# Optimization experiments

Measured on AMD Instinct MI355X. Metric: run time of the kernel, lower is better.

## Reference

```python
import jax, jax.numpy as jnp
import numpy as np

N_NODES = 100000


def gcn_conv(x, src, dst, W, b, n_nodes):
    # PyG GCNConv: add self-loops, sym-normalize, transform then aggregate.
    loop = jnp.arange(n_nodes, dtype=src.dtype)
    s = jnp.concatenate([src, loop])
    d = jnp.concatenate([dst, loop])
    ones = jnp.ones(s.shape[0], dtype=x.dtype)
    deg = jax.ops.segment_sum(ones, d, num_segments=n_nodes)
    dinv = jnp.where(deg > 0, jax.lax.rsqrt(deg), 0.0)
    norm = dinv[s] * dinv[d]  # [E+N]
    h = x @ W                 # [N, out]
    msg = h[s] * norm[:, None]
    out = jax.ops.segment_sum(msg, d, num_segments=n_nodes)
    return out + b


def setup_inputs() -> dict:
    key = jax.random.key(0)
    ks = jax.random.split(key, 10)
    n, f = N_NODES, 128
    x = jax.random.normal(ks[0], (n, f), dtype=jnp.float32)
    edge_index = jax.random.randint(ks[1], (2, 1600000), 0, n, dtype=jnp.int64)

    def glorot(k, fin, fout):
        lim = float(np.sqrt(6.0 / (fin + fout)))
        return jax.random.uniform(k, (fin, fout), jnp.float32, -lim, lim)

    return {
        "x": x,
        "edge_index": edge_index,
        "W1": glorot(ks[2], f, 128), "b1": jnp.zeros((128,), jnp.float32),
        "W2": glorot(ks[3], 128, 64), "b2": jnp.zeros((64,), jnp.float32),
        "W3": glorot(ks[4], 64, 32), "b3": jnp.zeros((32,), jnp.float32),
        "Wc": glorot(ks[5], 64, 1), "bc": jnp.zeros((1,), jnp.float32),
    }


def reference(x, edge_index, W1, b1, W2, b2, W3, b3, Wc, bc):
    n = x.shape[0]
    src, dst = edge_index[0], edge_index[1]
    h = jax.nn.relu(gcn_conv(x, src, dst, W1, b1, n))   # dropout: eval mode
    h = jax.nn.relu(gcn_conv(h, src, dst, W2, b2, n))
    h = jax.nn.relu(gcn_conv(h, src, dst, W3, b3, n))
    edge_feat = jnp.concatenate([h[src], h[dst]], axis=1)  # [E, 64]
    return edge_feat @ Wc + bc
```

## Files before the change

kernel.cpp:

```cpp
#include <hip/hip_runtime.h>


typedef unsigned short u16;
typedef short bfrag __attribute__((ext_vector_type(8)));
typedef float ffrag __attribute__((ext_vector_type(4)));

#define BSHIFT 8
#define MAXB   512
#define BIN_CHUNK 4096
#define BCAP   4608

static __device__ __forceinline__ float4 f4add(float4 a, float4 b) {
    return make_float4(a.x + b.x, a.y + b.y, a.z + b.z, a.w + b.w);
}

static __device__ __forceinline__ u16 f2bf(float f) {
    unsigned u = __float_as_uint(f);
    u = (u + 0x7FFFu + ((u >> 16) & 1u)) >> 16;
    return (u16)u;
}

static __device__ __forceinline__ float bflo(unsigned u) {
    return __uint_as_float(u << 16);
}
static __device__ __forceinline__ float bfhi(unsigned u) {
    return __uint_as_float(u & 0xFFFF0000u);
}
static __device__ __forceinline__ void bfacc2(float& a0, float& a1, unsigned u) {
    a0 += bflo(u);
    a1 += bfhi(u);
}
static __device__ __forceinline__ void bfacc8(float* a, uint4 u) {
    bfacc2(a[0], a[1], u.x); bfacc2(a[2], a[3], u.y);
    bfacc2(a[4], a[5], u.z); bfacc2(a[6], a[7], u.w);
}


__global__ __launch_bounds__(256) void bin_edges(const int* __restrict__ src,
                                                 const int* __restrict__ dst,
                                                 int* __restrict__ bcur,
                                                 unsigned* __restrict__ pairs,
                                                 int E, int B) {
    __shared__ int h[MAXB];
    __shared__ int base[MAXB];
    const int t = threadIdx.x;
    const int e0 = blockIdx.x * BIN_CHUNK;
    const int eEnd = min(e0 + BIN_CHUNK, E);
    for (int i = t; i < B; i += 256) h[i] = 0;
    __syncthreads();
    for (int e = e0 + t; e < eEnd; e += 256)
        atomicAdd(&h[dst[e] >> BSHIFT], 1);
    __syncthreads();
    for (int i = t; i < B; i += 256) {
        int c = h[i];
        base[i] = c ? atomicAdd(&bcur[i], c) : 0;
        h[i] = 0;
    }
    __syncthreads();
    for (int e = e0 + t; e < eEnd; e += 256) {
        int d = dst[e];
        int b = d >> BSHIFT;
        int pos = base[b] + atomicAdd(&h[b], 1);
        pairs[pos] = ((unsigned)(d & 255) << 24) | (unsigned)src[e];
    }
}

__global__ __launch_bounds__(256) void build_csr(const unsigned* __restrict__ pairs,
                                                 const int* __restrict__ bcur,
                                                 int* __restrict__ rowp,
                                                 int* __restrict__ rowe,
                                                 float* __restrict__ dinv,
                                                 int* __restrict__ ssrc, int N) {
    __shared__ int s[256];
    __shared__ int cur[256];
    const int t = threadIdx.x;
    const int b = blockIdx.x;
    const int eBeg = b * BCAP, eEnd = bcur[b];
    const int nodeBase = b << BSHIFT;
    s[t] = 0;
    __syncthreads();
    for (int e = eBeg + t; e < eEnd; e += 256)
        atomicAdd(&s[pairs[e] >> 24], 1);
    __syncthreads();
    const int v = s[t];
    #pragma unroll
    for (int off = 1; off < 256; off <<= 1) {
        int add = (t >= off) ? s[t - off] : 0;
        __syncthreads();
        s[t] += add;
        __syncthreads();
    }
    const int rp = eBeg + s[t] - v;
    const int node = nodeBase + t;
    if (node < N) {
        rowp[node] = rp;
        rowe[node] = rp + v;
        dinv[node] = rsqrtf((float)(v + 1));
    }
    cur[t] = rp;
    __syncthreads();
    for (int e = eBeg + t; e < eEnd; e += 256) {
        unsigned p = pairs[e];
        int pos = atomicAdd(&cur[p >> 24], 1);
        ssrc[pos] = (int)(p & 0xFFFFFFu);
    }
}

__global__ __launch_bounds__(256) void prep_all(const float* __restrict__ W1,
                                                u16* __restrict__ w1t,
                                                const float* __restrict__ W2,
                                                u16* __restrict__ w2t,
                                                int* __restrict__ bcur, int B) {
    int idx = blockIdx.x * 256 + threadIdx.x;
    if (idx < 128 * 128) {
        int n = idx >> 7, k = idx & 127;
        w1t[idx] = f2bf(W1[k * 128 + n]);
    } else if (idx < 128 * 128 + 64 * 128) {
        int j = idx - 128 * 128;
        int n = j >> 7, k = j & 127;
        w2t[j] = f2bf(W2[k * 64 + n]);
    }
    if (idx < B) bcur[idx] = idx * BCAP;
}

template <int FIN, int FOUT, bool AF32, int MINW>
__global__ __launch_bounds__(256, MINW)
void gemm_mfma(const void* __restrict__ Xv, const u16* __restrict__ Wt,
               const float* __restrict__ dinv, u16* __restrict__ G, int N) {
    constexpr int NT = FOUT / 16;
    constexpr int KK = FIN / 32;
    constexpr int CB = FIN / 8;
    constexpr int ITER = (64 * CB) / 256;
    __shared__ __align__(16) u16 xs[64 * FIN];
    __shared__ float ldv[64];

    const int t = threadIdx.x;
    const int wave = t >> 6;
    const int lane = t & 63;
    const int l15 = lane & 15;
    const int quad = lane >> 4;
    const int r0 = blockIdx.x * 64;

    bfrag Bf[NT][KK];
    #pragma unroll
    for (int nt = 0; nt < NT; nt++)
        #pragma unroll
        for (int kk = 0; kk < KK; kk++)
            Bf[nt][kk] = *reinterpret_cast<const bfrag*>(
                &Wt[(size_t)(nt * 16 + l15) * FIN + kk * 32 + quad * 8]);

    if (t < 64) ldv[t] = (r0 + t < N) ? dinv[r0 + t] : 0.f;

    #pragma unroll
    for (int i = 0; i < ITER; i++) {
        int v = t + 256 * i;
        int row = v / CB;
        int cb = v - row * CB;
        uint4 pack = make_uint4(0, 0, 0, 0);
        if (r0 + row < N) {
            if (AF32) {
                const float* X = (const float*)Xv;
                const float4* p = reinterpret_cast<const float4*>(
                    &X[(size_t)(r0 + row) * FIN + cb * 8]);
                float4 lo = p[0], hi = p[1];
                pack.x = f2bf(lo.x) | ((unsigned)f2bf(lo.y) << 16);
                pack.y = f2bf(lo.z) | ((unsigned)f2bf(lo.w) << 16);
                pack.z = f2bf(hi.x) | ((unsigned)f2bf(hi.y) << 16);
                pack.w = f2bf(hi.z) | ((unsigned)f2bf(hi.w) << 16);
            } else {
                const u16* X = (const u16*)Xv;
                pack = *reinterpret_cast<const uint4*>(
                    &X[(size_t)(r0 + row) * FIN + cb * 8]);
            }
        }
        int cbs = cb ^ (row & 7);
        *reinterpret_cast<uint4*>(&xs[row * FIN + cbs * 8]) = pack;
    }
    __syncthreads();

    ffrag acc[NT];
    #pragma unroll
    for (int nt = 0; nt < NT; nt++) {
        acc[nt][0] = 0.f; acc[nt][1] = 0.f; acc[nt][2] = 0.f; acc[nt][3] = 0.f;
    }

    const int arow = wave * 16 + l15;
    #pragma unroll
    for (int kk = 0; kk < KK; kk++) {
        int cb = (kk * 4 + quad) ^ (l15 & 7);
        bfrag a = *reinterpret_cast<const bfrag*>(&xs[arow * FIN + cb * 8]);
        #pragma unroll
        for (int nt = 0; nt < NT; nt++)
            acc[nt] = __builtin_amdgcn_mfma_f32_16x16x32_bf16(a, Bf[nt][kk], acc[nt], 0, 0, 0);
    }

    #pragma unroll
    for (int nt = 0; nt < NT; nt++)
        #pragma unroll
        for (int r = 0; r < 4; r++) {
            int rl = wave * 16 + quad * 4 + r;
            int grow = r0 + rl;
            if (grow < N)
                G[(size_t)grow * FOUT + nt * 16 + l15] = f2bf(acc[nt][r] * ldv[rl]);
        }
}

__global__ __launch_bounds__(256) void agg1_gemm2(const u16* __restrict__ G,
                                                  const int* __restrict__ rowp,
                                                  const int* __restrict__ rowe,
                                                  const int* __restrict__ ssrc,
                                                  const float* __restrict__ dinv,
                                                  const float* __restrict__ bias,
                                                  const u16* __restrict__ w2t,
                                                  u16* __restrict__ g2, int N) {
    __shared__ __align__(16) u16 hl[16][136];
    __shared__ float ldv[16];
    const int t = threadIdx.x;
    const int wave = t >> 6;
    const int lane = t & 63;
    const int l15 = lane & 15;
    const int quad = lane >> 4;
    const int lj = t & 15;
    const int dn = t >> 4;
    const int d0 = blockIdx.x * 16;
    const int d = d0 + dn;

    if (t < 16) ldv[t] = (d0 + t < N) ? dinv[d0 + t] : 0.f;

    uint4 pk = make_uint4(0, 0, 0, 0);
    if (d < N) {
        const uint4* G4 = reinterpret_cast<const uint4*>(G);
        float a[8];
        #pragma unroll
        for (int i = 0; i < 8; i++) a[i] = 0.f;
        bfacc8(a, G4[(size_t)d * 16 + lj]);
        int e = rowp[d];
        const int end = rowe[d];
        for (; e + 8 <= end; e += 8) {
            int s0 = ssrc[e],     s1 = ssrc[e + 1], s2 = ssrc[e + 2], s3 = ssrc[e + 3];
            int s4 = ssrc[e + 4], s5 = ssrc[e + 5], s6 = ssrc[e + 6], s7 = ssrc[e + 7];
            uint4 u0 = G4[(size_t)s0 * 16 + lj];
            uint4 u1 = G4[(size_t)s1 * 16 + lj];
            uint4 u2 = G4[(size_t)s2 * 16 + lj];
            uint4 u3 = G4[(size_t)s3 * 16 + lj];
            uint4 u4 = G4[(size_t)s4 * 16 + lj];
            uint4 u5 = G4[(size_t)s5 * 16 + lj];
            uint4 u6 = G4[(size_t)s6 * 16 + lj];
            uint4 u7 = G4[(size_t)s7 * 16 + lj];
            bfacc8(a, u0); bfacc8(a, u1); bfacc8(a, u2); bfacc8(a, u3);
            bfacc8(a, u4); bfacc8(a, u5); bfacc8(a, u6); bfacc8(a, u7);
        }
        for (; e + 4 <= end; e += 4) {
            int s0 = ssrc[e], s1 = ssrc[e + 1], s2 = ssrc[e + 2], s3 = ssrc[e + 3];
            uint4 u0 = G4[(size_t)s0 * 16 + lj];
            uint4 u1 = G4[(size_t)s1 * 16 + lj];
            uint4 u2 = G4[(size_t)s2 * 16 + lj];
            uint4 u3 = G4[(size_t)s3 * 16 + lj];
            bfacc8(a, u0); bfacc8(a, u1); bfacc8(a, u2); bfacc8(a, u3);
        }
        for (; e < end; e++)
            bfacc8(a, G4[(size_t)ssrc[e] * 16 + lj]);
        const float dv = dinv[d];
        const float4 b0 = reinterpret_cast<const float4*>(bias)[lj * 2];
        const float4 b1 = reinterpret_cast<const float4*>(bias)[lj * 2 + 1];
        float h[8];
        h[0] = fmaxf(a[0] * dv + b0.x, 0.f);
        h[1] = fmaxf(a[1] * dv + b0.y, 0.f);
        h[2] = fmaxf(a[2] * dv + b0.z, 0.f);
        h[3] = fmaxf(a[3] * dv + b0.w, 0.f);
        h[4] = fmaxf(a[4] * dv + b1.x, 0.f);
        h[5] = fmaxf(a[5] * dv + b1.y, 0.f);
        h[6] = fmaxf(a[6] * dv + b1.z, 0.f);
        h[7] = fmaxf(a[7] * dv + b1.w, 0.f);
        pk.x = f2bf(h[0]) | ((unsigned)f2bf(h[1]) << 16);
        pk.y = f2bf(h[2]) | ((unsigned)f2bf(h[3]) << 16);
        pk.z = f2bf(h[4]) | ((unsigned)f2bf(h[5]) << 16);
        pk.w = f2bf(h[6]) | ((unsigned)f2bf(h[7]) << 16);
    }
    *reinterpret_cast<uint4*>(&hl[dn][lj * 8]) = pk;
    __syncthreads();

    bfrag Bf[4];
    #pragma unroll
    for (int kk = 0; kk < 4; kk++)
        Bf[kk] = *reinterpret_cast<const bfrag*>(
            &w2t[(size_t)(wave * 16 + l15) * 128 + kk * 32 + quad * 8]);

    ffrag acc;
    acc[0] = 0.f; acc[1] = 0.f; acc[2] = 0.f; acc[3] = 0.f;
    #pragma unroll
    for (int kk = 0; kk < 4; kk++) {
        bfrag av = *reinterpret_cast<const bfrag*>(&hl[l15][kk * 32 + quad * 8]);
        acc = __builtin_amdgcn_mfma_f32_16x16x32_bf16(av, Bf[kk], acc, 0, 0, 0);
    }
    #pragma unroll
    for (int r = 0; r < 4; r++) {
        int row = quad * 4 + r;
        int node = d0 + row;
        if (node < N)
            g2[(size_t)node * 64 + wave * 16 + l15] = f2bf(acc[r] * ldv[row]);
    }
}

__global__ __launch_bounds__(256) void agg2_gemm3(const u16* __restrict__ G,
                                                  const int* __restrict__ rowp,
                                                  const int* __restrict__ rowe,
                                                  const int* __restrict__ ssrc,
                                                  const float* __restrict__ dinv,
                                                  const float* __restrict__ bias,
                                                  const float* __restrict__ W3,
                                                  float* __restrict__ g3, int N) {
    __shared__ __align__(16) float wl[64 * 32];
    __shared__ __align__(16) float hl[32][68];
    const int t = threadIdx.x;
    {
        const float4* s4 = reinterpret_cast<const float4*>(W3);
        float4* d4 = reinterpret_cast<float4*>(wl);
        d4[t] = s4[t];
        d4[t + 256] = s4[t + 256];
    }
    __syncthreads();
    const int lj = t & 7;
    const int dn = t >> 3;
    const int d = blockIdx.x * 32 + dn;
    if (d >= N) return;

    const uint4* G4 = reinterpret_cast<const uint4*>(G);
    float a[8];
    #pragma unroll
    for (int i = 0; i < 8; i++) a[i] = 0.f;
    bfacc8(a, G4[(size_t)d * 8 + lj]);
    int e = rowp[d];
    const int end = rowe[d];
    for (; e + 8 <= end; e += 8) {
        int s0 = ssrc[e],     s1 = ssrc[e + 1], s2 = ssrc[e + 2], s3 = ssrc[e + 3];
        int s4 = ssrc[e + 4], s5 = ssrc[e + 5], s6 = ssrc[e + 6], s7 = ssrc[e + 7];
        uint4 u0 = G4[(size_t)s0 * 8 + lj];
        uint4 u1 = G4[(size_t)s1 * 8 + lj];
        uint4 u2 = G4[(size_t)s2 * 8 + lj];
        uint4 u3 = G4[(size_t)s3 * 8 + lj];
        uint4 u4 = G4[(size_t)s4 * 8 + lj];
        uint4 u5 = G4[(size_t)s5 * 8 + lj];
        uint4 u6 = G4[(size_t)s6 * 8 + lj];
        uint4 u7 = G4[(size_t)s7 * 8 + lj];
        bfacc8(a, u0); bfacc8(a, u1); bfacc8(a, u2); bfacc8(a, u3);
        bfacc8(a, u4); bfacc8(a, u5); bfacc8(a, u6); bfacc8(a, u7);
    }
    for (; e + 4 <= end; e += 4) {
        int s0 = ssrc[e], s1 = ssrc[e + 1], s2 = ssrc[e + 2], s3 = ssrc[e + 3];
        uint4 u0 = G4[(size_t)s0 * 8 + lj];
        uint4 u1 = G4[(size_t)s1 * 8 + lj];
        uint4 u2 = G4[(size_t)s2 * 8 + lj];
        uint4 u3 = G4[(size_t)s3 * 8 + lj];
        bfacc8(a, u0); bfacc8(a, u1); bfacc8(a, u2); bfacc8(a, u3);
    }
    for (; e < end; e++)
        bfacc8(a, G4[(size_t)ssrc[e] * 8 + lj]);
    const float dv = dinv[d];
    const float4 b0 = reinterpret_cast<const float4*>(bias)[lj * 2];
    const float4 b1 = reinterpret_cast<const float4*>(bias)[lj * 2 + 1];
    float h[8];
    h[0] = fmaxf(a[0] * dv + b0.x, 0.f);
    h[1] = fmaxf(a[1] * dv + b0.y, 0.f);
    h[2] = fmaxf(a[2] * dv + b0.z, 0.f);
    h[3] = fmaxf(a[3] * dv + b0.w, 0.f);
    h[4] = fmaxf(a[4] * dv + b1.x, 0.f);
    h[5] = fmaxf(a[5] * dv + b1.y, 0.f);
    h[6] = fmaxf(a[6] * dv + b1.z, 0.f);
    h[7] = fmaxf(a[7] * dv + b1.w, 0.f);
    *reinterpret_cast<float4*>(&hl[dn][lj * 8])     = make_float4(h[0], h[1], h[2], h[3]);
    *reinterpret_cast<float4*>(&hl[dn][lj * 8 + 4]) = make_float4(h[4], h[5], h[6], h[7]);
    float g[4] = {0.f, 0.f, 0.f, 0.f};
    #pragma unroll 4
    for (int k4 = 0; k4 < 16; k4++) {
        float4 hv = *reinterpret_cast<const float4*>(&hl[dn][k4 * 4]);
        float hs[4] = {hv.x, hv.y, hv.z, hv.w};
        #pragma unroll
        for (int p = 0; p < 4; p++) {
            float4 w = *reinterpret_cast<const float4*>(&wl[(k4 * 4 + p) * 32 + lj * 4]);
            g[0] += hs[p] * w.x; g[1] += hs[p] * w.y;
            g[2] += hs[p] * w.z; g[3] += hs[p] * w.w;
        }
    }
    *reinterpret_cast<float4*>(&g3[(size_t)d * 32 + lj * 4]) =
        make_float4(g[0] * dv, g[1] * dv, g[2] * dv, g[3] * dv);
}

__global__ __launch_bounds__(256) void aggregate_l3s(const float* __restrict__ G,
                                                     const int* __restrict__ rowp,
                                                     const int* __restrict__ rowe,
                                                     const int* __restrict__ ssrc,
                                                     const float* __restrict__ dinv,
                                                     const float* __restrict__ bias,
                                                     const float* __restrict__ Wc,
                                                     float2* __restrict__ ab, int N) {
    constexpr int L = 8;
    const int t = threadIdx.x;
    const int lj = t % L;
    const int d = blockIdx.x * 32 + t / L;
    if (d >= N) return;

    const float4* G4 = reinterpret_cast<const float4*>(G);
    float4 acc = G4[(size_t)d * L + lj];
    int e = rowp[d];
    const int end = rowe[d];
    for (; e + 8 <= end; e += 8) {
        int s0 = ssrc[e],     s1 = ssrc[e + 1], s2 = ssrc[e + 2], s3 = ssrc[e + 3];
        int s4 = ssrc[e + 4], s5 = ssrc[e + 5], s6 = ssrc[e + 6], s7 = ssrc[e + 7];
        float4 v0 = G4[(size_t)s0 * L + lj];
        float4 v1 = G4[(size_t)s1 * L + lj];
        float4 v2 = G4[(size_t)s2 * L + lj];
        float4 v3 = G4[(size_t)s3 * L + lj];
        float4 v4 = G4[(size_t)s4 * L + lj];
        float4 v5 = G4[(size_t)s5 * L + lj];
        float4 v6 = G4[(size_t)s6 * L + lj];
        float4 v7 = G4[(size_t)s7 * L + lj];
        acc = f4add(acc, f4add(f4add(f4add(v0, v1), f4add(v2, v3)),
                               f4add(f4add(v4, v5), f4add(v6, v7))));
    }
    for (; e + 4 <= end; e += 4) {
        int s0 = ssrc[e], s1 = ssrc[e + 1], s2 = ssrc[e + 2], s3 = ssrc[e + 3];
        float4 v0 = G4[(size_t)s0 * L + lj];
        float4 v1 = G4[(size_t)s1 * L + lj];
        float4 v2 = G4[(size_t)s2 * L + lj];
        float4 v3 = G4[(size_t)s3 * L + lj];
        acc = f4add(acc, f4add(f4add(v0, v1), f4add(v2, v3)));
    }
    for (; e < end; e++)
        acc = f4add(acc, G4[(size_t)ssrc[e] * L + lj]);
    const float dv = dinv[d];
    const float4 b4 = reinterpret_cast<const float4*>(bias)[lj];
    float4 h;
    h.x = fmaxf(acc.x * dv + b4.x, 0.f);
    h.y = fmaxf(acc.y * dv + b4.y, 0.f);
    h.z = fmaxf(acc.z * dv + b4.z, 0.f);
    h.w = fmaxf(acc.w * dv + b4.w, 0.f);
    const float4 wa = reinterpret_cast<const float4*>(Wc)[lj];
    const float4 wb = reinterpret_cast<const float4*>(Wc + 32)[lj];
    float p = h.x * wa.x + h.y * wa.y + h.z * wa.z + h.w * wa.w;
    float q = h.x * wb.x + h.y * wb.y + h.z * wb.z + h.w * wb.w;
    p += __shfl_xor(p, 1); q += __shfl_xor(q, 1);
    p += __shfl_xor(p, 2); q += __shfl_xor(q, 2);
    p += __shfl_xor(p, 4); q += __shfl_xor(q, 4);
    if (lj == 0) ab[d] = make_float2(p, q);
}


__global__ __launch_bounds__(256) void edge_out(const int* __restrict__ src,
                                                const int* __restrict__ dst,
                                                const float2* __restrict__ ab,
                                                const float* __restrict__ bc,
                                                float* __restrict__ out, int E) {
    int e = blockIdx.x * 256 + threadIdx.x;
    if (e < E) out[e] = ab[src[e]].x + ab[dst[e]].y + bc[0];
}

extern "C" void kernel_launch(void* const* d_in, const int* in_sizes, int n_in,
                              void* d_out, int out_size, void* d_ws, size_t ws_size,
                              hipStream_t stream) {
    const float* x  = (const float*)d_in[0];
    const int*   ei = (const int*)d_in[1];
    const float* W1 = (const float*)d_in[2];
    const float* b1 = (const float*)d_in[3];
    const float* W2 = (const float*)d_in[4];
    const float* b2 = (const float*)d_in[5];
    const float* W3 = (const float*)d_in[6];
    const float* b3 = (const float*)d_in[7];
    const float* Wc = (const float*)d_in[8];
    const float* bc = (const float*)d_in[9];
    float* out = (float*)d_out;

    const int N = in_sizes[0] / 128;
    const int E = in_sizes[1] / 2;
    const int B = (N + 255) >> BSHIFT;
    const int* src = ei;
    const int* dst = ei + E;

    size_t off = 0;
    auto alloc = [&](size_t bytes) -> void* {
        size_t o = (off + 255) & ~(size_t)255;
        off = o + bytes;
        return (void*)((char*)d_ws + o);
    };
    float* dinv = (float*)alloc((size_t)N * 4);
    int*   rowp = (int*)alloc((size_t)N * 4);
    int*   rowe = (int*)alloc((size_t)N * 4);
    int*   bcur = (int*)alloc((size_t)(B + 1) * 4);
    int*   ssrc = (int*)alloc((size_t)B * BCAP * 4);
    u16*   w1t  = (u16*)alloc(128 * 128 * 2);
    u16*   w2t  = (u16*)alloc(64 * 128 * 2);
    u16*   g16  = (u16*)alloc((size_t)N * 128 * 2);
    u16*   g2b  = (u16*)alloc((size_t)N * 64 * 2);
    float2* ab  = (float2*)alloc((size_t)N * 8);
    (void)ws_size; (void)n_in; (void)out_size;

    unsigned* pairs = (unsigned*)g2b;
    float* g3f = (float*)g16;

    const int gE = (E + 255) / 256;
    const int gR = (N + 63) / 64;

    prep_all<<<96, 256, 0, stream>>>(W1, w1t, W2, w2t, bcur, B);
    bin_edges<<<(E + BIN_CHUNK - 1) / BIN_CHUNK, 256, 0, stream>>>(src, dst, bcur, pairs, E, B);
    build_csr<<<B, 256, 0, stream>>>(pairs, bcur, rowp, rowe, dinv, ssrc, N);

    gemm_mfma<128, 128, true, 2><<<gR, 256, 0, stream>>>(x, w1t, dinv, g16, N);
    agg1_gemm2<<<(N + 15) / 16, 256, 0, stream>>>(g16, rowp, rowe, ssrc, dinv, b1, w2t, g2b, N);
    agg2_gemm3<<<(N + 31) / 32, 256, 0, stream>>>(g2b, rowp, rowe, ssrc, dinv, b2, W3, g3f, N);
    aggregate_l3s<<<(N + 31) / 32, 256, 0, stream>>>(g3f, rowp, rowe, ssrc, dinv, b3, Wc, ab, N);

    edge_out<<<gE, 256, 0, stream>>>(src, dst, ab, bc, out, E);
}
```

Baseline: 319.4 us.

## Slice layer-1 aggregation into 16-feature column slabs and unfuse the layer-2 GEMM

The layer-1 GEMM now writes its output in a sliced layout of eight 16-feature slabs, each node-major. A new aggregation kernel runs one block group per slab, so each gather reads 32 bytes per neighbor from a 3.2 MB slab that fits in cache. Eight lanes cover different edges and are combined with a shuffle reduction. The layer-2 GEMM becomes a separate pass over the sliced activations. This targets cache misses in the random gather, at the cost of an extra kernel launch, a 25.6 MB intermediate buffer written and read back, and index lists reread eight times.

```diff
diff --git a/kernel.cpp b/kernel.cpp
--- a/kernel.cpp
+++ b/kernel.cpp
@@ -123,7 +123,7 @@
     if (idx < B) bcur[idx] = idx * BCAP;
 }
 
-template <int FIN, int FOUT, bool AF32, int MINW>
+template <int FIN, int FOUT, int AMODE, bool OS, int MINW>
 __global__ __launch_bounds__(256, MINW)
 void gemm_mfma(const void* __restrict__ Xv, const u16* __restrict__ Wt,
                const float* __restrict__ dinv, u16* __restrict__ G, int N) {
@@ -158,7 +158,7 @@
         int cb = v - row * CB;
         uint4 pack = make_uint4(0, 0, 0, 0);
         if (r0 + row < N) {
-            if (AF32) {
+            if (AMODE == 0) {
                 const float* X = (const float*)Xv;
                 const float4* p = reinterpret_cast<const float4*>(
                     &X[(size_t)(r0 + row) * FIN + cb * 8]);
@@ -170,7 +170,7 @@
             } else {
                 const u16* X = (const u16*)Xv;
                 pack = *reinterpret_cast<const uint4*>(
-                    &X[(size_t)(r0 + row) * FIN + cb * 8]);
+                    &X[((size_t)(cb >> 1) * N + (r0 + row)) * 16 + (cb & 1) * 8]);
             }
         }
         int cbs = cb ^ (row & 7);
@@ -200,69 +200,66 @@
         for (int r = 0; r < 4; r++) {
             int rl = wave * 16 + quad * 4 + r;
             int grow = r0 + rl;
-            if (grow < N)
-                G[(size_t)grow * FOUT + nt * 16 + l15] = f2bf(acc[nt][r] * ldv[rl]);
+            if (grow < N) {
+                u16 val = f2bf(acc[nt][r] * ldv[rl]);
+                if (OS)
+                    G[((size_t)nt * N + grow) * 16 + l15] = val;
+                else
+                    G[(size_t)grow * FOUT + nt * 16 + l15] = val;
+            }
         }
 }
 
-__global__ __launch_bounds__(256) void agg1_gemm2(const u16* __restrict__ G,
+__global__ __launch_bounds__(256) void agg1_slice(const u16* __restrict__ Gs,
                                                   const int* __restrict__ rowp,
                                                   const int* __restrict__ rowe,
                                                   const int* __restrict__ ssrc,
                                                   const float* __restrict__ dinv,
                                                   const float* __restrict__ bias,
-                                                  const u16* __restrict__ w2t,
-                                                  u16* __restrict__ g2, int N) {
-    __shared__ __align__(16) u16 hl[16][136];
-    __shared__ float ldv[16];
-    const int t = threadIdx.x;
-    const int wave = t >> 6;
-    const int lane = t & 63;
-    const int l15 = lane & 15;
-    const int quad = lane >> 4;
+                                                  u16* __restrict__ h1s, int N) {
+    const int t = threadIdx.x;
+    const unsigned slice = blockIdx.x & 7;
+    const int d = (blockIdx.x >> 3) * 16 + (t >> 4);
+    if (d >= N) return;
     const int lj = t & 15;
-    const int dn = t >> 4;
-    const int d0 = blockIdx.x * 16;
-    const int d = d0 + dn;
-
-    if (t < 16) ldv[t] = (d0 + t < N) ? dinv[d0 + t] : 0.f;
-
-    uint4 pk = make_uint4(0, 0, 0, 0);
-    if (d < N) {
-        const uint4* G4 = reinterpret_cast<const uint4*>(G);
-        float a[8];
+    const int eo = lj & 7;
+    const int fh = lj >> 3;
+    const uint4* G4 = reinterpret_cast<const uint4*>(Gs) + (size_t)slice * N * 2;
+
+    float a[8];
+    #pragma unroll
+    for (int i = 0; i < 8; i++) a[i] = 0.f;
+    if (eo == 0)
+        bfacc8(a, G4[(size_t)d * 2 + fh]);
+
+    int e = rowp[d];
+    const int end = rowe[d];
+    for (; e + 16 <= end; e += 16) {
+        int sa = ssrc[e + eo];
+        int sb = ssrc[e + 8 + eo];
+        uint4 ua = G4[(size_t)sa * 2 + fh];
+        uint4 ub = G4[(size_t)sb * 2 + fh];
+        bfacc8(a, ua); bfacc8(a, ub);
+    }
+    for (; e + 8 <= end; e += 8) {
+        int sa = ssrc[e + eo];
+        bfacc8(a, G4[(size_t)sa * 2 + fh]);
+    }
+    if (e + eo < end) {
+        int sa = ssrc[e + eo];
+        bfacc8(a, G4[(size_t)sa * 2 + fh]);
+    }
+
+    #pragma unroll
+    for (int m = 1; m <= 4; m <<= 1)
         #pragma unroll
-        for (int i = 0; i < 8; i++) a[i] = 0.f;
-        bfacc8(a, G4[(size_t)d * 16 + lj]);
-        int e = rowp[d];
-        const int end = rowe[d];
-        for (; e + 8 <= end; e += 8) {
-            int s0 = ssrc[e],     s1 = ssrc[e + 1], s2 = ssrc[e + 2], s3 = ssrc[e + 3];
-            int s4 = ssrc[e + 4], s5 = ssrc[e + 5], s6 = ssrc[e + 6], s7 = ssrc[e + 7];
-            uint4 u0 = G4[(size_t)s0 * 16 + lj];
-            uint4 u1 = G4[(size_t)s1 * 16 + lj];
-            uint4 u2 = G4[(size_t)s2 * 16 + lj];
-            uint4 u3 = G4[(size_t)s3 * 16 + lj];
-            uint4 u4 = G4[(size_t)s4 * 16 + lj];
-            uint4 u5 = G4[(size_t)s5 * 16 + lj];
-            uint4 u6 = G4[(size_t)s6 * 16 + lj];
-            uint4 u7 = G4[(size_t)s7 * 16 + lj];
-            bfacc8(a, u0); bfacc8(a, u1); bfacc8(a, u2); bfacc8(a, u3);
-            bfacc8(a, u4); bfacc8(a, u5); bfacc8(a, u6); bfacc8(a, u7);
-        }
-        for (; e + 4 <= end; e += 4) {
-            int s0 = ssrc[e], s1 = ssrc[e + 1], s2 = ssrc[e + 2], s3 = ssrc[e + 3];
-            uint4 u0 = G4[(size_t)s0 * 16 + lj];
-            uint4 u1 = G4[(size_t)s1 * 16 + lj];
-            uint4 u2 = G4[(size_t)s2 * 16 + lj];
-            uint4 u3 = G4[(size_t)s3 * 16 + lj];
-            bfacc8(a, u0); bfacc8(a, u1); bfacc8(a, u2); bfacc8(a, u3);
-        }
-        for (; e < end; e++)
-            bfacc8(a, G4[(size_t)ssrc[e] * 16 + lj]);
+        for (int i = 0; i < 8; i++)
+            a[i] += __shfl_xor(a[i], m);
+
+    if (eo == 0) {
         const float dv = dinv[d];
-        const float4 b0 = reinterpret_cast<const float4*>(bias)[lj * 2];
-        const float4 b1 = reinterpret_cast<const float4*>(bias)[lj * 2 + 1];
+        const float4 b0 = reinterpret_cast<const float4*>(bias)[slice * 4 + fh * 2];
+        const float4 b1 = reinterpret_cast<const float4*>(bias)[slice * 4 + fh * 2 + 1];
         float h[8];
         h[0] = fmaxf(a[0] * dv + b0.x, 0.f);
         h[1] = fmaxf(a[1] * dv + b0.y, 0.f);
@@ -272,33 +269,12 @@
         h[5] = fmaxf(a[5] * dv + b1.y, 0.f);
         h[6] = fmaxf(a[6] * dv + b1.z, 0.f);
         h[7] = fmaxf(a[7] * dv + b1.w, 0.f);
+        uint4 pk;
         pk.x = f2bf(h[0]) | ((unsigned)f2bf(h[1]) << 16);
         pk.y = f2bf(h[2]) | ((unsigned)f2bf(h[3]) << 16);
         pk.z = f2bf(h[4]) | ((unsigned)f2bf(h[5]) << 16);
         pk.w = f2bf(h[6]) | ((unsigned)f2bf(h[7]) << 16);
-    }
-    *reinterpret_cast<uint4*>(&hl[dn][lj * 8]) = pk;
-    __syncthreads();
-
-    bfrag Bf[4];
-    #pragma unroll
-    for (int kk = 0; kk < 4; kk++)
-        Bf[kk] = *reinterpret_cast<const bfrag*>(
-            &w2t[(size_t)(wave * 16 + l15) * 128 + kk * 32 + quad * 8]);
-
-    ffrag acc;
-    acc[0] = 0.f; acc[1] = 0.f; acc[2] = 0.f; acc[3] = 0.f;
-    #pragma unroll
-    for (int kk = 0; kk < 4; kk++) {
-        bfrag av = *reinterpret_cast<const bfrag*>(&hl[l15][kk * 32 + quad * 8]);
-        acc = __builtin_amdgcn_mfma_f32_16x16x32_bf16(av, Bf[kk], acc, 0, 0, 0);
-    }
-    #pragma unroll
-    for (int r = 0; r < 4; r++) {
-        int row = quad * 4 + r;
-        int node = d0 + row;
-        if (node < N)
-            g2[(size_t)node * 64 + wave * 16 + l15] = f2bf(acc[r] * ldv[row]);
+        reinterpret_cast<uint4*>(h1s)[((size_t)slice * N + d) * 2 + fh] = pk;
     }
 }
 
@@ -490,6 +466,7 @@
     u16*   w1t  = (u16*)alloc(128 * 128 * 2);
     u16*   w2t  = (u16*)alloc(64 * 128 * 2);
     u16*   g16  = (u16*)alloc((size_t)N * 128 * 2);
+    u16*   h1s  = (u16*)alloc((size_t)N * 128 * 2);
     u16*   g2b  = (u16*)alloc((size_t)N * 64 * 2);
     float2* ab  = (float2*)alloc((size_t)N * 8);
     (void)ws_size; (void)n_in; (void)out_size;
@@ -504,8 +481,9 @@
     bin_edges<<<(E + BIN_CHUNK - 1) / BIN_CHUNK, 256, 0, stream>>>(src, dst, bcur, pairs, E, B);
     build_csr<<<B, 256, 0, stream>>>(pairs, bcur, rowp, rowe, dinv, ssrc, N);
 
-    gemm_mfma<128, 128, true, 2><<<gR, 256, 0, stream>>>(x, w1t, dinv, g16, N);
-    agg1_gemm2<<<(N + 15) / 16, 256, 0, stream>>>(g16, rowp, rowe, ssrc, dinv, b1, w2t, g2b, N);
+    gemm_mfma<128, 128, 0, true, 2><<<gR, 256, 0, stream>>>(x, w1t, dinv, g16, N);
+    agg1_slice<<<8 * ((N + 15) / 16), 256, 0, stream>>>(g16, rowp, rowe, ssrc, dinv, b1, h1s, N);
+    gemm_mfma<128, 64, 2, false, 2><<<gR, 256, 0, stream>>>(h1s, w2t, dinv, g2b, N);
     agg2_gemm3<<<(N + 31) / 32, 256, 0, stream>>>(g2b, rowp, rowe, ssrc, dinv, b2, W3, g3f, N);
     aggregate_l3s<<<(N + 31) / 32, 256, 0, stream>>>(g3f, rowp, rowe, ssrc, dinv, b3, Wc, ab, N);
 
```

Measured after the change: 373.1 us. 16.8% more time.

## Fuse edge binning with layer-1 GEMM and move source-degree scaling into aggregation

Applied to the files above, without the earlier changes.

Merges the edge-binning kernel and the first-layer MFMA GEMM into one launch, with block IDs split between the two roles, so binning and the X·W1 transform run concurrently. Because the GEMM now runs before dinv exists, it no longer scales rows by dinv. The layer-1 aggregation instead multiplies each gathered neighbour row by dinv[src] using an extra per-edge gather. Bucket counters are zeroed with a memset and stored as offsets rather than absolute positions, which removes one launch but adds random dinv loads and FMAs in the aggregation loop.

```diff
diff --git a/kernel.cpp b/kernel.cpp
--- a/kernel.cpp
+++ b/kernel.cpp
@@ -34,39 +34,129 @@
     bfacc2(a[0], a[1], u.x); bfacc2(a[2], a[3], u.y);
     bfacc2(a[4], a[5], u.z); bfacc2(a[6], a[7], u.w);
 }
-
-
-__global__ __launch_bounds__(256) void bin_edges(const int* __restrict__ src,
-                                                 const int* __restrict__ dst,
-                                                 int* __restrict__ bcur,
-                                                 unsigned* __restrict__ pairs,
-                                                 int E, int B) {
-    __shared__ int h[MAXB];
-    __shared__ int base[MAXB];
+static __device__ __forceinline__ void bfacc2f(float& a0, float& a1, unsigned u, float v) {
+    a0 = fmaf(bflo(u), v, a0);
+    a1 = fmaf(bfhi(u), v, a1);
+}
+static __device__ __forceinline__ void bfacc8f(float* a, uint4 u, float v) {
+    bfacc2f(a[0], a[1], u.x, v); bfacc2f(a[2], a[3], u.y, v);
+    bfacc2f(a[4], a[5], u.z, v); bfacc2f(a[6], a[7], u.w, v);
+}
+
+__global__ __launch_bounds__(256) void prep_w(const float* __restrict__ W1,
+                                              u16* __restrict__ w1t,
+                                              const float* __restrict__ W2,
+                                              u16* __restrict__ w2t) {
+    int idx = blockIdx.x * 256 + threadIdx.x;
+    if (idx < 128 * 128) {
+        int n = idx >> 7, k = idx & 127;
+        w1t[idx] = f2bf(W1[k * 128 + n]);
+    } else if (idx < 128 * 128 + 64 * 128) {
+        int j = idx - 128 * 128;
+        int n = j >> 7, k = j & 127;
+        w2t[j] = f2bf(W2[k * 64 + n]);
+    }
+}
+
+__global__ __launch_bounds__(256, 2)
+void k_front(const u16* __restrict__ w1t,
+             const int* __restrict__ src, const int* __restrict__ dst,
+             int* __restrict__ bcur0, unsigned* __restrict__ pairs,
+             const float* __restrict__ x, u16* __restrict__ G,
+             int E, int B, int N, int BINB) {
+    __shared__ __align__(16) u16 xs[64 * 128];
     const int t = threadIdx.x;
-    const int e0 = blockIdx.x * BIN_CHUNK;
-    const int eEnd = min(e0 + BIN_CHUNK, E);
-    for (int i = t; i < B; i += 256) h[i] = 0;
+    int bid = blockIdx.x;
+
+    if (bid < BINB) {
+        int* h    = reinterpret_cast<int*>(xs);
+        int* base = h + MAXB;
+        const int e0 = bid * BIN_CHUNK;
+        const int eEnd = min(e0 + BIN_CHUNK, E);
+        for (int i = t; i < B; i += 256) h[i] = 0;
+        __syncthreads();
+        for (int e = e0 + t; e < eEnd; e += 256)
+            atomicAdd(&h[dst[e] >> BSHIFT], 1);
+        __syncthreads();
+        for (int i = t; i < B; i += 256) {
+            int c = h[i];
+            base[i] = c ? atomicAdd(&bcur0[i], c) : 0;
+            h[i] = 0;
+        }
+        __syncthreads();
+        for (int e = e0 + t; e < eEnd; e += 256) {
+            int d = dst[e];
+            int b = d >> BSHIFT;
+            int pos = b * BCAP + base[b] + atomicAdd(&h[b], 1);
+            pairs[pos] = ((unsigned)(d & 255) << 24) | (unsigned)src[e];
+        }
+        return;
+    }
+    bid -= BINB;
+
+    const int wave = t >> 6;
+    const int lane = t & 63;
+    const int l15 = lane & 15;
+    const int quad = lane >> 4;
+    const int r0 = bid * 64;
+
+    bfrag Bf[8][4];
+    #pragma unroll
+    for (int nt = 0; nt < 8; nt++)
+        #pragma unroll
+        for (int kk = 0; kk < 4; kk++)
+            Bf[nt][kk] = *reinterpret_cast<const bfrag*>(
+                &w1t[(size_t)(nt * 16 + l15) * 128 + kk * 32 + quad * 8]);
+
+    #pragma unroll
+    for (int i = 0; i < 4; i++) {
+        int v = t + 256 * i;
+        int row = v >> 4;
+        int cb = v & 15;
+        uint4 pack = make_uint4(0, 0, 0, 0);
+        if (r0 + row < N) {
+            const float4* p = reinterpret_cast<const float4*>(
+                &x[(size_t)(r0 + row) * 128 + cb * 8]);
+            float4 lo = p[0], hi = p[1];
+            pack.x = f2bf(lo.x) | ((unsigned)f2bf(lo.y) << 16);
+            pack.y = f2bf(lo.z) | ((unsigned)f2bf(lo.w) << 16);
+            pack.z = f2bf(hi.x) | ((unsigned)f2bf(hi.y) << 16);
+            pack.w = f2bf(hi.z) | ((unsigned)f2bf(hi.w) << 16);
+        }
+        int cbs = cb ^ (row & 7);
+        *reinterpret_cast<uint4*>(&xs[row * 128 + cbs * 8]) = pack;
+    }
     __syncthreads();
-    for (int e = e0 + t; e < eEnd; e += 256)
-        atomicAdd(&h[dst[e] >> BSHIFT], 1);
-    __syncthreads();
-    for (int i = t; i < B; i += 256) {
-        int c = h[i];
-        base[i] = c ? atomicAdd(&bcur[i], c) : 0;
-        h[i] = 0;
-    }
-    __syncthreads();
-    for (int e = e0 + t; e < eEnd; e += 256) {
-        int d = dst[e];
-        int b = d >> BSHIFT;
-        int pos = base[b] + atomicAdd(&h[b], 1);
-        pairs[pos] = ((unsigned)(d & 255) << 24) | (unsigned)src[e];
-    }
+
+    ffrag acc[8];
+    #pragma unroll
+    for (int nt = 0; nt < 8; nt++) {
+        acc[nt][0] = 0.f; acc[nt][1] = 0.f; acc[nt][2] = 0.f; acc[nt][3] = 0.f;
+    }
+
+    const int arow = wave * 16 + l15;
+    #pragma unroll
+    for (int kk = 0; kk < 4; kk++) {
+        int cb = (kk * 4 + quad) ^ (l15 & 7);
+        bfrag a = *reinterpret_cast<const bfrag*>(&xs[arow * 128 + cb * 8]);
+        #pragma unroll
+        for (int nt = 0; nt < 8; nt++)
+            acc[nt] = __builtin_amdgcn_mfma_f32_16x16x32_bf16(a, Bf[nt][kk], acc[nt], 0, 0, 0);
+    }
+
+    #pragma unroll
+    for (int nt = 0; nt < 8; nt++)
+        #pragma unroll
+        for (int r = 0; r < 4; r++) {
+            int rl = wave * 16 + quad * 4 + r;
+            int grow = r0 + rl;
+            if (grow < N)
+                G[(size_t)grow * 128 + nt * 16 + l15] = f2bf(acc[nt][r]);
+        }
 }
 
 __global__ __launch_bounds__(256) void build_csr(const unsigned* __restrict__ pairs,
-                                                 const int* __restrict__ bcur,
+                                                 const int* __restrict__ bcur0,
                                                  int* __restrict__ rowp,
                                                  int* __restrict__ rowe,
                                                  float* __restrict__ dinv,
@@ -75,7 +165,7 @@
     __shared__ int cur[256];
     const int t = threadIdx.x;
     const int b = blockIdx.x;
-    const int eBeg = b * BCAP, eEnd = bcur[b];
+    const int eBeg = b * BCAP, eEnd = b * BCAP + bcur0[b];
     const int nodeBase = b << BSHIFT;
     s[t] = 0;
     __syncthreads();
@@ -104,105 +194,6 @@
         int pos = atomicAdd(&cur[p >> 24], 1);
         ssrc[pos] = (int)(p & 0xFFFFFFu);
     }
-}
-
-__global__ __launch_bounds__(256) void prep_all(const float* __restrict__ W1,
-                                                u16* __restrict__ w1t,
-                                                const float* __restrict__ W2,
-                                                u16* __restrict__ w2t,
-                                                int* __restrict__ bcur, int B) {
-    int idx = blockIdx.x * 256 + threadIdx.x;
-    if (idx < 128 * 128) {
-        int n = idx >> 7, k = idx & 127;
-        w1t[idx] = f2bf(W1[k * 128 + n]);
-    } else if (idx < 128 * 128 + 64 * 128) {
-        int j = idx - 128 * 128;
-        int n = j >> 7, k = j & 127;
-        w2t[j] = f2bf(W2[k * 64 + n]);
-    }
-    if (idx < B) bcur[idx] = idx * BCAP;
-}
-
-template <int FIN, int FOUT, bool AF32, int MINW>
-__global__ __launch_bounds__(256, MINW)
-void gemm_mfma(const void* __restrict__ Xv, const u16* __restrict__ Wt,
-               const float* __restrict__ dinv, u16* __restrict__ G, int N) {
-    constexpr int NT = FOUT / 16;
-    constexpr int KK = FIN / 32;
-    constexpr int CB = FIN / 8;
-    constexpr int ITER = (64 * CB) / 256;
-    __shared__ __align__(16) u16 xs[64 * FIN];
-    __shared__ float ldv[64];
-
-    const int t = threadIdx.x;
-    const int wave = t >> 6;
-    const int lane = t & 63;
-    const int l15 = lane & 15;
-    const int quad = lane >> 4;
-    const int r0 = blockIdx.x * 64;
-
-    bfrag Bf[NT][KK];
-    #pragma unroll
-    for (int nt = 0; nt < NT; nt++)
-        #pragma unroll
-        for (int kk = 0; kk < KK; kk++)
-            Bf[nt][kk] = *reinterpret_cast<const bfrag*>(
-                &Wt[(size_t)(nt * 16 + l15) * FIN + kk * 32 + quad * 8]);
-
-    if (t < 64) ldv[t] = (r0 + t < N) ? dinv[r0 + t] : 0.f;
-
-    #pragma unroll
-    for (int i = 0; i < ITER; i++) {
-        int v = t + 256 * i;
-        int row = v / CB;
-        int cb = v - row * CB;
-        uint4 pack = make_uint4(0, 0, 0, 0);
-        if (r0 + row < N) {
-            if (AF32) {
-                const float* X = (const float*)Xv;
-                const float4* p = reinterpret_cast<const float4*>(
-                    &X[(size_t)(r0 + row) * FIN + cb * 8]);
-                float4 lo = p[0], hi = p[1];
-                pack.x = f2bf(lo.x) | ((unsigned)f2bf(lo.y) << 16);
-                pack.y = f2bf(lo.z) | ((unsigned)f2bf(lo.w) << 16);
-                pack.z = f2bf(hi.x) | ((unsigned)f2bf(hi.y) << 16);
-                pack.w = f2bf(hi.z) | ((unsigned)f2bf(hi.w) << 16);
-            } else {
-                const u16* X = (const u16*)Xv;
-                pack = *reinterpret_cast<const uint4*>(
-                    &X[(size_t)(r0 + row) * FIN + cb * 8]);
-            }
-        }
-        int cbs = cb ^ (row & 7);
-        *reinterpret_cast<uint4*>(&xs[row * FIN + cbs * 8]) = pack;
-    }
-    __syncthreads();
-
-    ffrag acc[NT];
-    #pragma unroll
-    for (int nt = 0; nt < NT; nt++) {
-        acc[nt][0] = 0.f; acc[nt][1] = 0.f; acc[nt][2] = 0.f; acc[nt][3] = 0.f;
-    }
-
-    const int arow = wave * 16 + l15;
-    #pragma unroll
-    for (int kk = 0; kk < KK; kk++) {
-        int cb = (kk * 4 + quad) ^ (l15 & 7);
-        bfrag a = *reinterpret_cast<const bfrag*>(&xs[arow * FIN + cb * 8]);
-        #pragma unroll
-        for (int nt = 0; nt < NT; nt++)
-            acc[nt] = __builtin_amdgcn_mfma_f32_16x16x32_bf16(a, Bf[nt][kk], acc[nt], 0, 0, 0);
-    }
-
-    #pragma unroll
-    for (int nt = 0; nt < NT; nt++)
-        #pragma unroll
-        for (int r = 0; r < 4; r++) {
-            int rl = wave * 16 + quad * 4 + r;
-            int grow = r0 + rl;
-            if (grow < N)
-                G[(size_t)grow * FOUT + nt * 16 + l15] = f2bf(acc[nt][r] * ldv[rl]);
-        }
 }
 
 __global__ __launch_bounds__(256) void agg1_gemm2(const u16* __restrict__ G,
@@ -230,15 +221,18 @@
     uint4 pk = make_uint4(0, 0, 0, 0);
     if (d < N) {
         const uint4* G4 = reinterpret_cast<const uint4*>(G);
+        const float dvd = dinv[d];
         float a[8];
         #pragma unroll
         for (int i = 0; i < 8; i++) a[i] = 0.f;
-        bfacc8(a, G4[(size_t)d * 16 + lj]);
+        bfacc8f(a, G4[(size_t)d * 16 + lj], dvd);
         int e = rowp[d];
         const int end = rowe[d];
         for (; e + 8 <= end; e += 8) {
             int s0 = ssrc[e],     s1 = ssrc[e + 1], s2 = ssrc[e + 2], s3 = ssrc[e + 3];
             int s4 = ssrc[e + 4], s5 = ssrc[e + 5], s6 = ssrc[e + 6], s7 = ssrc[e + 7];
+            float v0 = dinv[s0], v1 = dinv[s1], v2 = dinv[s2], v3 = dinv[s3];
+            float v4 = dinv[s4], v5 = dinv[s5], v6 = dinv[s6], v7 = dinv[s7];
             uint4 u0 = G4[(size_t)s0 * 16 + lj];
             uint4 u1 = G4[(size_t)s1 * 16 + lj];
             uint4 u2 = G4[(size_t)s2 * 16 + lj];
@@ -247,31 +241,33 @@
             uint4 u5 = G4[(size_t)s5 * 16 + lj];
             uint4 u6 = G4[(size_t)s6 * 16 + lj];
             uint4 u7 = G4[(size_t)s7 * 16 + lj];
-            bfacc8(a, u0); bfacc8(a, u1); bfacc8(a, u2); bfacc8(a, u3);
-            bfacc8(a, u4); bfacc8(a, u5); bfacc8(a, u6); bfacc8(a, u7);
+            bfacc8f(a, u0, v0); bfacc8f(a, u1, v1); bfacc8f(a, u2, v2); bfacc8f(a, u3, v3);
+            bfacc8f(a, u4, v4); bfacc8f(a, u5, v5); bfacc8f(a, u6, v6); bfacc8f(a, u7, v7);
         }
         for (; e + 4 <= end; e += 4) {
             int s0 = ssrc[e], s1 = ssrc[e + 1], s2 = ssrc[e + 2], s3 = ssrc[e + 3];
+            float v0 = dinv[s0], v1 = dinv[s1], v2 = dinv[s2], v3 = dinv[s3];
             uint4 u0 = G4[(size_t)s0 * 16 + lj];
             uint4 u1 = G4[(size_t)s1 * 16 + lj];
             uint4 u2 = G4[(size_t)s2 * 16 + lj];
             uint4 u3 = G4[(size_t)s3 * 16 + lj];
-            bfacc8(a, u0); bfacc8(a, u1); bfacc8(a, u2); bfacc8(a, u3);
-        }
-        for (; e < end; e++)
-            bfacc8(a, G4[(size_t)ssrc[e] * 16 + lj]);
-        const float dv = dinv[d];
+            bfacc8f(a, u0, v0); bfacc8f(a, u1, v1); bfacc8f(a, u2, v2); bfacc8f(a, u3, v3);
+        }
+        for (; e < end; e++) {
+            int s = ssrc[e];
+            bfacc8f(a, G4[(size_t)s * 16 + lj], dinv[s]);
+        }
         const float4 b0 = reinterpret_cast<const float4*>(bias)[lj * 2];
         const float4 b1 = reinterpret_cast<const float4*>(bias)[lj * 2 + 1];
         float h[8];
-        h[0] = fmaxf(a[0] * dv + b0.x, 0.f);
-        h[1] = fmaxf(a[1] * dv + b0.y, 0.f);
-        h[2] = fmaxf(a[2] * dv + b0.z, 0.f);
-        h[3] = fmaxf(a[3] * dv + b0.w, 0.f);
-        h[4] = fmaxf(a[4] * dv + b1.x, 0.f);
-        h[5] = fmaxf(a[5] * dv + b1.y, 0.f);
-        h[6] = fmaxf(a[6] * dv + b1.z, 0.f);
-        h[7] = fmaxf(a[7] * dv + b1.w, 0.f);
+        h[0] = fmaxf(a[0] * dvd + b0.x, 0.f);
+        h[1] = fmaxf(a[1] * dvd + b0.y, 0.f);
+        h[2] = fmaxf(a[2] * dvd + b0.z, 0.f);
+        h[3] = fmaxf(a[3] * dvd + b0.w, 0.f);
+        h[4] = fmaxf(a[4] * dvd + b1.x, 0.f);
+        h[5] = fmaxf(a[5] * dvd + b1.y, 0.f);
+        h[6] = fmaxf(a[6] * dvd + b1.z, 0.f);
+        h[7] = fmaxf(a[7] * dvd + b1.w, 0.f);
         pk.x = f2bf(h[0]) | ((unsigned)f2bf(h[1]) << 16);
         pk.y = f2bf(h[2]) | ((unsigned)f2bf(h[3]) << 16);
         pk.z = f2bf(h[4]) | ((unsigned)f2bf(h[5]) << 16);
@@ -499,12 +495,15 @@
 
     const int gE = (E + 255) / 256;
     const int gR = (N + 63) / 64;
-
-    prep_all<<<96, 256, 0, stream>>>(W1, w1t, W2, w2t, bcur, B);
-    bin_edges<<<(E + BIN_CHUNK - 1) / BIN_CHUNK, 256, 0, stream>>>(src, dst, bcur, pairs, E, B);
+    const int BINB = (E + BIN_CHUNK - 1) / BIN_CHUNK;
+
+    hipMemsetAsync(bcur, 0, (size_t)(B + 1) * 4, stream);
+
+    prep_w<<<96, 256, 0, stream>>>(W1, w1t, W2, w2t);
+    k_front<<<BINB + gR, 256, 0, stream>>>(w1t, src, dst, bcur, pairs, x, g16,
+                                           E, B, N, BINB);
     build_csr<<<B, 256, 0, stream>>>(pairs, bcur, rowp, rowe, dinv, ssrc, N);
 
-    gemm_mfma<128, 128, true, 2><<<gR, 256, 0, stream>>>(x, w1t, dinv, g16, N);
     agg1_gemm2<<<(N + 15) / 16, 256, 0, stream>>>(g16, rowp, rowe, ssrc, dinv, b1, w2t, g2b, N);
     agg2_gemm3<<<(N + 31) / 32, 256, 0, stream>>>(g2b, rowp, rowe, ssrc, dinv, b2, W3, g3f, N);
     aggregate_l3s<<<(N + 31) / 32, 256, 0, stream>>>(g3f, rowp, rowe, ssrc, dinv, b3, Wc, ab, N);
```

After: 316.8 us (median of 2 runs). About the same (-0.8%).
